# Kernel tuning notes

Hardware: AMD Instinct MI355X
Metric: run time of the kernel (lower is better)

Reference implementation:

```python
import jax, jax.numpy as jnp
import numpy as np

NEG_SLOPE = 0.2  # PyG GATConv default leaky_relu slope


def _gat_layer(x, W, att_src, att_dst, bias, src, dst, num_nodes, heads, out_c, concat):
    # x: [N, F_in] -> h: [N, H, C]
    h = (x @ W).reshape(num_nodes, heads, out_c)
    a_src = jnp.einsum('nhc,hc->nh', h, att_src)  # [N, H]
    a_dst = jnp.einsum('nhc,hc->nh', h, att_dst)  # [N, H]
    # edge (src -> dst): attention logit per edge/head
    e = jax.nn.leaky_relu(a_src[src] + a_dst[dst], NEG_SLOPE)  # [E, H]
    # softmax over edges sharing the same destination node
    m = jax.ops.segment_max(e, dst, num_segments=num_nodes)  # [N, H]
    m = jnp.where(jnp.isfinite(m), m, 0.0)
    ex = jnp.exp(e - m[dst])
    denom = jax.ops.segment_sum(ex, dst, num_segments=num_nodes)  # [N, H]
    alpha = ex / (denom[dst] + 1e-16)  # [E, H]
    # weighted scatter-add aggregation
    msg = h[src] * alpha[:, :, None]  # [E, H, C]
    out = jax.ops.segment_sum(msg, dst, num_segments=num_nodes)  # [N, H, C]
    if concat:
        out = out.reshape(num_nodes, heads * out_c)
    else:
        out = out.mean(axis=1)
    return out + bias


def _add_self_loops(edge_index, num_nodes):
    loop = jnp.arange(num_nodes, dtype=edge_index.dtype)
    src = jnp.concatenate([edge_index[0], loop])
    dst = jnp.concatenate([edge_index[1], loop])
    return src, dst


def setup_inputs() -> dict:
    key = jax.random.key(0)
    ks = jax.random.split(key, 9)
    N, F_in, E, H, C, OUT = 30000, 256, 300000, 8, 128, 64
    x = jax.random.normal(ks[0], (N, F_in), dtype=jnp.float32)
    edge_index = jax.random.randint(ks[1], (2, E), 0, N, dtype=jnp.int32)
    s1 = 1.0 / np.sqrt(F_in)
    s2 = 1.0 / np.sqrt(H * C)
    return {
        'x': x,
        'edge_index': edge_index,
        'W1': jax.random.normal(ks[2], (F_in, H * C), dtype=jnp.float32) * s1,
        'att_src1': jax.random.normal(ks[3], (H, C), dtype=jnp.float32) * s2,
        'att_dst1': jax.random.normal(ks[4], (H, C), dtype=jnp.float32) * s2,
        'b1': jnp.zeros((H * C,), dtype=jnp.float32),
        'W2': jax.random.normal(ks[5], (H * C, OUT), dtype=jnp.float32) * s2,
        'att_src2': jax.random.normal(ks[6], (1, OUT), dtype=jnp.float32) * 0.125,
        'att_dst2': jax.random.normal(ks[7], (1, OUT), dtype=jnp.float32) * 0.125,
        'b2': jnp.zeros((OUT,), dtype=jnp.float32),
    }


def reference(x, edge_index, W1, att_src1, att_dst1, b1, W2, att_src2, att_dst2, b2):
    N = x.shape[0]
    src, dst = _add_self_loops(edge_index, N)
    # dropout layers are identity in eval mode
    h = _gat_layer(x, W1, att_src1, att_dst1, b1, src, dst, N, 8, 128, True)
    h = jax.nn.elu(h)
    out = _gat_layer(h, W2, att_src2, att_dst2, b2, src, dst, N, 1, 64, False)
    return jax.nn.log_softmax(out, axis=-1)
```

## Files before the change

kernel.cpp:

```cpp
#include <hip/hip_runtime.h>
#include <math.h>

#define N_NODES 30000
#define F_IN 256
#define E_RAW 300000
#define E_TOT (E_RAW + N_NODES)
#define HEADS 8
#define CH 128
#define HC 1024
#define OUTC 64
#define NEG_SLOPE 0.2f
#define CAP 64

typedef __attribute__((ext_vector_type(8))) short bf16x8;
typedef __attribute__((ext_vector_type(4))) float f32x4;
typedef __attribute__((ext_vector_type(2))) float f32x2;

__device__ __forceinline__ float bf2f(unsigned short u) {
    return __uint_as_float(((unsigned)u) << 16);
}
__device__ __forceinline__ unsigned short f2bf(float f) {
    unsigned b = __float_as_uint(f);
    b += 0x7FFFu + ((b >> 16) & 1u);
    return (unsigned short)(b >> 16);
}
__device__ __forceinline__ void edge_sd(const int* __restrict__ ei, int e, int& s, int& d) {
    if (e < E_RAW) { s = ei[e]; d = ei[E_RAW + e]; }
    else           { s = e - E_RAW; d = s; }
}
__device__ __forceinline__ void async_cp16(const void* g, void* l) {
    __builtin_amdgcn_global_load_lds((const __attribute__((address_space(1))) void*)g,
                                     (__attribute__((address_space(3))) void*)l, 16, 0, 0);
}
__device__ __forceinline__ int slotP(int s) {
    return ((s >> 6) << 6) + ((s >> 2) & 15) + ((s & 3) << 4);
}
__device__ __forceinline__ void wave_sync() {
    __builtin_amdgcn_fence(__ATOMIC_ACQ_REL, "wavefront");
    __builtin_amdgcn_wave_barrier();
}

#define NB_CVTX (N_NODES * F_IN / 4 / 256)
#define NB_DEG  ((E_TOT + 255) / 256)
#define NB_W1T  ((F_IN * HC + 255) / 256)
#define NB_W2T  ((HC * OUTC + 255) / 256)
#define NB_PREP (NB_CVTX + NB_DEG + NB_W1T + NB_W2T)

__global__ __launch_bounds__(256)
void prep_kernel(const float* __restrict__ x, unsigned short* __restrict__ xb,
                 const float* __restrict__ W1, unsigned short* __restrict__ W1t,
                 const float* __restrict__ W2, unsigned short* __restrict__ W2t,
                 const int* __restrict__ ei, int* __restrict__ deg)
{
    const int b = blockIdx.x, t = threadIdx.x;
    if (b < NB_CVTX) {
        int i = b * 256 + t;
        const float4 v = reinterpret_cast<const float4*>(x)[i];
        ushort4 o;
        o.x = f2bf(v.x); o.y = f2bf(v.y); o.z = f2bf(v.z); o.w = f2bf(v.w);
        reinterpret_cast<ushort4*>(xb)[i] = o;
    } else if (b < NB_CVTX + NB_DEG) {
        int e = (b - NB_CVTX) * 256 + t;
        if (e < E_TOT) {
            int s, d; edge_sd(ei, e, s, d);
            atomicAdd(&deg[d], 1);
        }
    } else if (b < NB_CVTX + NB_DEG + NB_W1T) {
        int i = (b - NB_CVTX - NB_DEG) * 256 + t;
        if (i < F_IN * HC) {
            int k = i >> 10, n = i & (HC - 1);
            W1t[n * F_IN + k] = f2bf(W1[i]);
        }
    } else {
        int i = (b - NB_CVTX - NB_DEG - NB_W1T) * 256 + t;
        if (i < HC * OUTC) {
            int s = i >> 6, n = i & (OUTC - 1);
            W2t[n * HC + s] = f2bf(W2[slotP(s) * OUTC + n]);
        }
    }
}

__global__ __launch_bounds__(256)
void gemm1_mfma(const unsigned short* __restrict__ A,
                const unsigned short* __restrict__ Bt,
                unsigned* __restrict__ Cp,
                const float* __restrict__ att_src, const float* __restrict__ att_dst,
                float* __restrict__ a_src, float* __restrict__ a_dst, int M)
{
    __shared__ unsigned short Al[128 * 64];
    __shared__ unsigned short Bl[128 * 64];
    __shared__ float s_src[128][2];
    __shared__ float s_dst[128][2];
    const int tid  = threadIdx.x;
    const int wave = tid >> 6, lane = tid & 63;
    const int quad = lane >> 4, l16 = lane & 15;
    const int wr = (wave >> 1) * 64, wc = (wave & 1) * 64;
    const int row0 = blockIdx.y * 128;
    const int col0 = blockIdx.x * 128;

    f32x4 acc[4][4];
#pragma unroll
    for (int i = 0; i < 4; i++)
#pragma unroll
        for (int j = 0; j < 4; j++) acc[i][j] = (f32x4){0.f, 0.f, 0.f, 0.f};

    for (int k0 = 0; k0 < F_IN; k0 += 64) {
#pragma unroll
        for (int p = 0; p < 4; p++) {
            int idx = tid + 256 * p;
            int r = idx >> 3, q = idx & 7;
            async_cp16(A + (size_t)(row0 + r) * F_IN + k0 + ((q ^ (r & 7)) * 8),
                       Al + (size_t)(wave * 64 + 256 * p) * 8);
        }
#pragma unroll
        for (int p = 0; p < 4; p++) {
            int idx = tid + 256 * p;
            int r = idx >> 3, q = idx & 7;
            async_cp16(Bt + (size_t)(col0 + r) * F_IN + k0 + ((q ^ (r & 7)) * 8),
                       Bl + (size_t)(wave * 64 + 256 * p) * 8);
        }
        __syncthreads();
#pragma unroll
        for (int kh = 0; kh < 2; kh++) {
            const int cx = (kh * 4 + quad) ^ (l16 & 7);
            bf16x8 af[4], bg[4];
#pragma unroll
            for (int i = 0; i < 4; i++)
                af[i] = *reinterpret_cast<const bf16x8*>(Al + ((wr + i * 16 + l16) * 8 + cx) * 8);
#pragma unroll
            for (int j = 0; j < 4; j++)
                bg[j] = *reinterpret_cast<const bf16x8*>(Bl + ((wc + j * 16 + l16) * 8 + cx) * 8);
#pragma unroll
            for (int i = 0; i < 4; i++)
#pragma unroll
                for (int j = 0; j < 4; j++)
                    acc[i][j] = __builtin_amdgcn_mfma_f32_16x16x32_bf16(af[i], bg[j], acc[i][j], 0, 0, 0);
        }
        __syncthreads();
    }
    const int D = ((col0 + wc) >> 6) * 16 + l16;
#pragma unroll
    for (int i = 0; i < 4; i++) {
#pragma unroll
        for (int r = 0; r < 4; r++) {
            int row = row0 + wr + i * 16 + quad * 4 + r;
            if (row >= M) continue;
            int w8 = __builtin_amdgcn_cvt_pk_fp8_f32(acc[i][0][r], acc[i][1][r], 0, false);
            w8 = __builtin_amdgcn_cvt_pk_fp8_f32(acc[i][2][r], acc[i][3][r], w8, true);
            Cp[(size_t)row * 256 + D] = (unsigned)w8;
        }
    }
    const float* asv = att_src + blockIdx.x * CH;
    const float* adv = att_dst + blockIdx.x * CH;
    float av[4], dv[4];
#pragma unroll
    for (int j = 0; j < 4; j++) {
        av[j] = asv[wc + j * 16 + l16];
        dv[j] = adv[wc + j * 16 + l16];
    }
#pragma unroll
    for (int i = 0; i < 4; i++) {
#pragma unroll
        for (int r = 0; r < 4; r++) {
            float ps = 0.f, pd = 0.f;
#pragma unroll
            for (int j = 0; j < 4; j++) {
                float cc = acc[i][j][r];
                ps += cc * av[j];
                pd += cc * dv[j];
            }
#pragma unroll
            for (int o = 1; o < 16; o <<= 1) {
                ps += __shfl_xor(ps, o);
                pd += __shfl_xor(pd, o);
            }
            if (l16 == 0) {
                int lr = wr + i * 16 + quad * 4 + r;
                s_src[lr][wc >> 6] = ps;
                s_dst[lr][wc >> 6] = pd;
            }
        }
    }
    __syncthreads();
    if (tid < 128) {
        int row = row0 + tid;
        if (row < M) {
            a_src[row * 8 + blockIdx.x] = s_src[tid][0] + s_src[tid][1];
            a_dst[row * 8 + blockIdx.x] = s_dst[tid][0] + s_dst[tid][1];
        }
    }
}

__global__ __launch_bounds__(256)
void gemm2_mfma(const unsigned short* __restrict__ A,
                const unsigned short* __restrict__ Bt,
                unsigned short* __restrict__ C,
                const float* __restrict__ att_src2, const float* __restrict__ att_dst2,
                float* __restrict__ a_src2, float* __restrict__ a_dst2, int M)
{
    __shared__ unsigned short Al[64 * 64];
    __shared__ unsigned short Bl[64 * 64];
    const int tid  = threadIdx.x;
    const int wave = tid >> 6, lane = tid & 63;
    const int quad = lane >> 4, l16 = lane & 15;
    const int wr = wave * 16;
    const int row0 = blockIdx.x * 64;

    f32x4 acc[4];
#pragma unroll
    for (int j = 0; j < 4; j++) acc[j] = (f32x4){0.f, 0.f, 0.f, 0.f};

    for (int k0 = 0; k0 < HC; k0 += 64) {
#pragma unroll
        for (int p = 0; p < 2; p++) {
            int idx = tid + 256 * p;
            int r = idx >> 3, q = idx & 7;
            async_cp16(A + (size_t)(row0 + r) * HC + k0 + ((q ^ (r & 7)) * 8),
                       Al + (size_t)(wave * 64 + 256 * p) * 8);
        }
#pragma unroll
        for (int p = 0; p < 2; p++) {
            int idx = tid + 256 * p;
            int r = idx >> 3, q = idx & 7;
            async_cp16(Bt + (size_t)r * HC + k0 + ((q ^ (r & 7)) * 8),
                       Bl + (size_t)(wave * 64 + 256 * p) * 8);
        }
        __syncthreads();
#pragma unroll
        for (int kh = 0; kh < 2; kh++) {
            const int cx = (kh * 4 + quad) ^ (l16 & 7);
            bf16x8 af, bg[4];
            af = *reinterpret_cast<const bf16x8*>(Al + ((wr + l16) * 8 + cx) * 8);
#pragma unroll
            for (int j = 0; j < 4; j++)
                bg[j] = *reinterpret_cast<const bf16x8*>(Bl + ((j * 16 + l16) * 8 + cx) * 8);
#pragma unroll
            for (int j = 0; j < 4; j++)
                acc[j] = __builtin_amdgcn_mfma_f32_16x16x32_bf16(af, bg[j], acc[j], 0, 0, 0);
        }
        __syncthreads();
    }
    float av[4], dv[4];
#pragma unroll
    for (int j = 0; j < 4; j++) {
        av[j] = att_src2[j * 16 + l16];
        dv[j] = att_dst2[j * 16 + l16];
    }
#pragma unroll
    for (int r = 0; r < 4; r++) {
        int row = row0 + wr + quad * 4 + r;
        float ps = 0.f, pd = 0.f;
#pragma unroll
        for (int j = 0; j < 4; j++) {
            float cc = acc[j][r];
            int col = j * 16 + l16;
            if (row < M) C[(size_t)row * OUTC + col] = f2bf(cc);
            ps += cc * av[j];
            pd += cc * dv[j];
        }
#pragma unroll
        for (int o = 1; o < 16; o <<= 1) {
            ps += __shfl_xor(ps, o);
            pd += __shfl_xor(pd, o);
        }
        if (l16 == 0 && row < M) {
            a_src2[row] = ps;
            a_dst2[row] = pd;
        }
    }
}

__global__ __launch_bounds__(256)
void alloc_kernel(const int* __restrict__ deg, int* __restrict__ rowstart,
                  int* __restrict__ cursor, int* __restrict__ counter)
{
    int d = blockIdx.x * 256 + threadIdx.x;
    int lane = threadIdx.x & 63;
    int v = (d < N_NODES) ? deg[d] : 0;
    int x = v;
#pragma unroll
    for (int o = 1; o < 64; o <<= 1) {
        int y = __shfl_up(x, o);
        if (lane >= o) x += y;
    }
    int excl = x - v;
    int total = __shfl(x, 63);
    int base = 0;
    if (lane == 63) base = atomicAdd(counter, total);
    base = __shfl(base, 63);
    if (d < N_NODES) {
        rowstart[d] = base + excl;
        cursor[d]   = base + excl;
    }
}

__global__ void scatter_kernel(const int* __restrict__ ei, int* __restrict__ cursor,
                               int* __restrict__ csr_src)
{
    int e = blockIdx.x * 256 + threadIdx.x;
    if (e >= E_TOT) return;
    int s, d; edge_sd(ei, e, s, d);
    int pos = atomicAdd(&cursor[d], 1);
    csr_src[pos] = s;
}

__global__ __launch_bounds__(256)
void agg1_fused(const int* __restrict__ rowstart, const int* __restrict__ degv,
                const int* __restrict__ csr_src,
                const unsigned* __restrict__ h1p,
                const float* __restrict__ a_src1, const float* __restrict__ a_dst1,
                const float* __restrict__ b1, unsigned short* __restrict__ out1)
{
    const int t   = threadIdx.x;
    const int sub = t >> 6;
    const int tl  = t & 63;
    const int h   = tl >> 3;
    const int d   = blockIdx.x * 4 + sub;

    __shared__ float exps[4][CAP * 8];
    __shared__ int   srcs[4][CAP];

    const int start = rowstart[d];
    const int deg   = degv[d];

    const float adst = a_dst1[d * 8 + h];
    const uint4* __restrict__ h1v = reinterpret_cast<const uint4*>(h1p);

    float denom_part = 0.f;
    float acc[16];
#pragma unroll
    for (int k = 0; k < 16; k++) acc[k] = 0.f;

    for (int c0 = 0; c0 < deg; c0 += CAP) {
        const int cend = min(deg - c0, CAP);
        for (int c = (tl & 7); c < cend; c += 8) {
            int s = csr_src[start + c0 + c];
            if (h == 0) srcs[sub][c] = s;
            float a = a_src1[s * 8 + h] + adst;
            float v = a > 0.f ? a : NEG_SLOPE * a;
            float ex = __expf(v);
            exps[sub][c * 8 + h] = ex;
            denom_part += ex;
        }
        wave_sync();
        {
            int   s_cur = srcs[sub][0];
            float w_cur = exps[sub][h];
            uint4 u_cur = h1v[(size_t)s_cur * 64 + tl];
            for (int c = 0; c < cend; c++) {
                int   s_nxt = 0; float w_nxt = 0.f; uint4 u_nxt;
                if (c + 1 < cend) {
                    s_nxt = srcs[sub][c + 1];
                    w_nxt = exps[sub][(c + 1) * 8 + h];
                    u_nxt = h1v[(size_t)s_nxt * 64 + tl];
                }
#pragma unroll
                for (int dw = 0; dw < 4; dw++) {
                    unsigned wd = (&u_cur.x)[dw];
                    f32x2 lo = __builtin_amdgcn_cvt_pk_f32_fp8((int)wd, false);
                    f32x2 hi = __builtin_amdgcn_cvt_pk_f32_fp8((int)wd, true);
                    acc[dw * 4 + 0] += w_cur * lo.x;
                    acc[dw * 4 + 1] += w_cur * lo.y;
                    acc[dw * 4 + 2] += w_cur * hi.x;
                    acc[dw * 4 + 3] += w_cur * hi.y;
                }
                s_cur = s_nxt; w_cur = w_nxt; u_cur = u_nxt;
            }
        }
        wave_sync();
    }
#pragma unroll
    for (int o = 1; o < 8; o <<= 1) denom_part += __shfl_xor(denom_part, o);
    const float dinv = 1.f / (denom_part + 1e-16f);

    unsigned short ov[16];
#pragma unroll
    for (int e = 0; e < 16; e++) {
        float v = acc[e] * dinv + b1[slotP(16 * tl + e)];
        v = v > 0.f ? v : __expf(v) - 1.f;
        ov[e] = f2bf(v);
    }
    uint4* op = reinterpret_cast<uint4*>(out1 + (size_t)d * HC + 16 * tl);
    op[0] = *reinterpret_cast<uint4*>(&ov[0]);
    op[1] = *reinterpret_cast<uint4*>(&ov[8]);
}

__global__ __launch_bounds__(256)
void agg2_lsm(const int* __restrict__ rowstart, const int* __restrict__ degv,
              const int* __restrict__ csr_src,
              const unsigned short* __restrict__ h2,
              const float* __restrict__ a_src2, const float* __restrict__ a_dst2,
              const float* __restrict__ b2, float* __restrict__ out)
{
    const int t = threadIdx.x;
    const int sub  = t >> 6;
    const int lane = t & 63;
    const int eo   = lane >> 4;
    const int cq   = lane & 15;
    const int d = blockIdx.x * 4 + sub;

    __shared__ float exs[4][CAP];
    __shared__ int   ss[4][CAP];

    const int start = rowstart[d];
    const int deg   = degv[d];

    const float adst = a_dst2[d];
    const uint2* __restrict__ h2v = reinterpret_cast<const uint2*>(h2);
    float denom_part = 0.f;
    float ax = 0.f, ay = 0.f, az = 0.f, aw = 0.f;

    for (int c0 = 0; c0 < deg; c0 += CAP) {
        const int cend = min(deg - c0, CAP);
        for (int c = lane; c < cend; c += 64) {
            int s = csr_src[start + c0 + c];
            ss[sub][c] = s;
            float a = a_src2[s] + adst;
            float v = a > 0.f ? a : NEG_SLOPE * a;
            float ex = __expf(v);
            exs[sub][c] = ex;
            denom_part += ex;
        }
        wave_sync();
        {
            int   cc = eo;
            float w0 = (cc < cend) ? exs[sub][cc] : 0.f;
            int   s0 = (cc < cend) ? ss[sub][cc] : ss[sub][0];
            uint2 u0 = h2v[(size_t)s0 * 16 + cq];
            for (int c = 0; c + 4 < cend; c += 4) {
                int cc1 = c + 4 + eo;
                float w1 = (cc1 < cend) ? exs[sub][cc1] : 0.f;
                int   s1 = (cc1 < cend) ? ss[sub][cc1] : ss[sub][0];
                uint2 u1 = h2v[(size_t)s1 * 16 + cq];
                ax += w0 * __uint_as_float(u0.x << 16);
                ay += w0 * __uint_as_float(u0.x & 0xFFFF0000u);
                az += w0 * __uint_as_float(u0.y << 16);
                aw += w0 * __uint_as_float(u0.y & 0xFFFF0000u);
                w0 = w1; s0 = s1; u0 = u1;
            }
            ax += w0 * __uint_as_float(u0.x << 16);
            ay += w0 * __uint_as_float(u0.x & 0xFFFF0000u);
            az += w0 * __uint_as_float(u0.y << 16);
            aw += w0 * __uint_as_float(u0.y & 0xFFFF0000u);
        }
        wave_sync();
    }
    ax += __shfl_xor(ax, 16); ax += __shfl_xor(ax, 32);
    ay += __shfl_xor(ay, 16); ay += __shfl_xor(ay, 32);
    az += __shfl_xor(az, 16); az += __shfl_xor(az, 32);
    aw += __shfl_xor(aw, 16); aw += __shfl_xor(aw, 32);
#pragma unroll
    for (int o = 32; o > 0; o >>= 1) denom_part += __shfl_xor(denom_part, o);
    const float dinv = 1.f / (denom_part + 1e-16f);

    float4 bb = reinterpret_cast<const float4*>(b2)[cq];
    float v0 = ax * dinv + bb.x;
    float v1 = ay * dinv + bb.y;
    float v2 = az * dinv + bb.z;
    float v3 = aw * dinv + bb.w;
    float m = fmaxf(fmaxf(v0, v1), fmaxf(v2, v3));
#pragma unroll
    for (int o = 1; o < 16; o <<= 1) m = fmaxf(m, __shfl_xor(m, o));
    float ex = __expf(v0 - m) + __expf(v1 - m) + __expf(v2 - m) + __expf(v3 - m);
    float ssum = ex;
#pragma unroll
    for (int o = 1; o < 16; o <<= 1) ssum += __shfl_xor(ssum, o);
    if (eo == 0) {
        float lg = __logf(ssum);
        reinterpret_cast<float4*>(out + (size_t)d * OUTC)[cq] =
            make_float4(v0 - m - lg, v1 - m - lg, v2 - m - lg, v3 - m - lg);
    }
}

extern "C" void kernel_launch(void* const* d_in, const int* in_sizes, int n_in,
                              void* d_out, int out_size, void* d_ws, size_t ws_size,
                              hipStream_t stream)
{
    const float* x   = (const float*)d_in[0];
    const int*   ei  = (const int*)d_in[1];
    const float* W1  = (const float*)d_in[2];
    const float* as1 = (const float*)d_in[3];
    const float* ad1 = (const float*)d_in[4];
    const float* b1  = (const float*)d_in[5];
    const float* W2  = (const float*)d_in[6];
    const float* as2 = (const float*)d_in[7];
    const float* ad2 = (const float*)d_in[8];
    const float* b2  = (const float*)d_in[9];

    char* p = (char*)d_ws;
    auto alloc = [&](size_t bytes) { char* r = p; p += (bytes + 255) & ~(size_t)255; return r; };

    char* region0 = (char*)alloc((size_t)N_NODES * HC * 2);
    unsigned* h1p = (unsigned*)region0;

    char* region1 = (char*)alloc((size_t)N_NODES * HC * 2);
    unsigned short* out1 = (unsigned short*)region1;
    unsigned short* xb   = (unsigned short*)region1;
    unsigned short* W1t  = (unsigned short*)(region1 + (size_t)N_NODES * F_IN * 2 + 256);

    unsigned short* W2t = (unsigned short*)alloc((size_t)OUTC * HC * 2);

    float* a_src1   = (float*)alloc((size_t)N_NODES * HEADS * 4);
    float* a_dst1   = (float*)alloc((size_t)N_NODES * HEADS * 4);
    int*   deg      = (int*)alloc((size_t)(N_NODES + 1) * 4);
    int*   counter  = deg + N_NODES;
    int*   rowstart = (int*)alloc((size_t)N_NODES * 4);
    int*   cursor   = (int*)alloc((size_t)N_NODES * 4);
    int*   csr_src  = (int*)alloc((size_t)E_TOT * 4);

    char* q = region0;
    auto alias = [&](size_t bytes) { char* r = q; q += (bytes + 255) & ~(size_t)255; return r; };
    unsigned short* h2 = (unsigned short*)alias((size_t)N_NODES * OUTC * 2);
    float* a_src2  = (float*)alias((size_t)N_NODES * 4);
    float* a_dst2  = (float*)alias((size_t)N_NODES * 4);

    hipMemsetAsync(deg, 0, (size_t)(N_NODES + 1) * 4, stream);

    prep_kernel<<<NB_PREP, 256, 0, stream>>>(x, xb, W1, W1t, W2, W2t, ei, deg);

    alloc_kernel<<<(N_NODES + 255) / 256, 256, 0, stream>>>(deg, rowstart, cursor, counter);
    scatter_kernel<<<(E_TOT + 255) / 256, 256, 0, stream>>>(ei, cursor, csr_src);

    gemm1_mfma<<<dim3(HC / 128, (N_NODES + 127) / 128), 256, 0, stream>>>(
        xb, W1t, h1p, as1, ad1, a_src1, a_dst1, N_NODES);
    agg1_fused<<<N_NODES / 4, 256, 0, stream>>>(rowstart, deg, csr_src, h1p, a_src1, a_dst1, b1, out1);

    gemm2_mfma<<<(N_NODES + 63) / 64, 256, 0, stream>>>(
        out1, W2t, h2, as2, ad2, a_src2, a_dst2, N_NODES);
    agg2_lsm<<<N_NODES / 4, 256, 0, stream>>>(rowstart, deg, csr_src, h2, a_src2, a_dst2, b2, (float*)d_out);
}
```

Measured before the change: 259.0 us.

## Stream agg1 edges with 4-wide register prefetch, dropping shared-memory staging

The layer-1 aggregation no longer runs a two-phase scheme that first computes per-edge exp weights into shared memory and then replays them. Each wave now walks the CSR row in groups of four edges, software-pipelined one group ahead for the feature and logit loads and two groups ahead for the source indices. Each lane recomputes its head's exp weight inline, so the wave syncs, the LDS traffic and the shuffle reduction of the denominator go away. The row start and degree are made wave-uniform with readfirstlane. The cost is redundant exp and logit loads across the 8 lanes that share a head, plus higher register pressure from holding eight uint4 loads in flight.

```diff
diff --git a/kernel.cpp b/kernel.cpp
--- a/kernel.cpp
+++ b/kernel.cpp
@@ -304,6 +304,55 @@
     csr_src[pos] = s;
 }
 
+struct SG4 { int s0, s1, s2, s3; };
+struct AU4 { float a0, a1, a2, a3; uint4 u0, u1, u2, u3; };
+
+__device__ __forceinline__ SG4 ld_s4(const int* __restrict__ csr_src,
+                                     int start, int base, int deg)
+{
+    SG4 g;
+    g.s0 = (base + 0 < deg) ? csr_src[start + base + 0] : -1;
+    g.s1 = (base + 1 < deg) ? csr_src[start + base + 1] : -1;
+    g.s2 = (base + 2 < deg) ? csr_src[start + base + 2] : -1;
+    g.s3 = (base + 3 < deg) ? csr_src[start + base + 3] : -1;
+    return g;
+}
+
+__device__ __forceinline__ AU4 ld_au4(const float* __restrict__ a_src1,
+                                      const uint4* __restrict__ h1v,
+                                      SG4 g, int h, int tl)
+{
+    AU4 r;
+    const uint4 z = make_uint4(0u, 0u, 0u, 0u);
+    if (g.s0 >= 0) { r.a0 = a_src1[g.s0 * 8 + h]; r.u0 = h1v[(size_t)g.s0 * 64 + tl]; }
+    else           { r.a0 = -1e30f; r.u0 = z; }
+    if (g.s1 >= 0) { r.a1 = a_src1[g.s1 * 8 + h]; r.u1 = h1v[(size_t)g.s1 * 64 + tl]; }
+    else           { r.a1 = -1e30f; r.u1 = z; }
+    if (g.s2 >= 0) { r.a2 = a_src1[g.s2 * 8 + h]; r.u2 = h1v[(size_t)g.s2 * 64 + tl]; }
+    else           { r.a2 = -1e30f; r.u2 = z; }
+    if (g.s3 >= 0) { r.a3 = a_src1[g.s3 * 8 + h]; r.u3 = h1v[(size_t)g.s3 * 64 + tl]; }
+    else           { r.a3 = -1e30f; r.u3 = z; }
+    return r;
+}
+
+#define AGG1_DW(wd_, k_) do { \
+    f32x2 lo_ = __builtin_amdgcn_cvt_pk_f32_fp8((int)(wd_), false); \
+    f32x2 hi_ = __builtin_amdgcn_cvt_pk_f32_fp8((int)(wd_), true);  \
+    acc[(k_) + 0] += w_ * lo_.x; \
+    acc[(k_) + 1] += w_ * lo_.y; \
+    acc[(k_) + 2] += w_ * hi_.x; \
+    acc[(k_) + 3] += w_ * hi_.y; \
+} while (0)
+
+#define AGG1_EDGE(aa, uu) do { \
+    float al_ = (aa) + adst; \
+    float v_ = al_ > 0.f ? al_ : NEG_SLOPE * al_; \
+    float w_ = __expf(v_); \
+    denom += w_; \
+    AGG1_DW((uu).x, 0); AGG1_DW((uu).y, 4); \
+    AGG1_DW((uu).z, 8); AGG1_DW((uu).w, 12); \
+} while (0)
+
 __global__ __launch_bounds__(256)
 void agg1_fused(const int* __restrict__ rowstart, const int* __restrict__ degv,
                 const int* __restrict__ csr_src,
@@ -317,61 +366,32 @@
     const int h   = tl >> 3;
     const int d   = blockIdx.x * 4 + sub;
 
-    __shared__ float exps[4][CAP * 8];
-    __shared__ int   srcs[4][CAP];
-
-    const int start = rowstart[d];
-    const int deg   = degv[d];
-
+    const int start = __builtin_amdgcn_readfirstlane(rowstart[d]);
+    const int deg   = __builtin_amdgcn_readfirstlane(degv[d]);
     const float adst = a_dst1[d * 8 + h];
     const uint4* __restrict__ h1v = reinterpret_cast<const uint4*>(h1p);
 
-    float denom_part = 0.f;
+    float denom = 0.f;
     float acc[16];
 #pragma unroll
     for (int k = 0; k < 16; k++) acc[k] = 0.f;
 
-    for (int c0 = 0; c0 < deg; c0 += CAP) {
-        const int cend = min(deg - c0, CAP);
-        for (int c = (tl & 7); c < cend; c += 8) {
-            int s = csr_src[start + c0 + c];
-            if (h == 0) srcs[sub][c] = s;
-            float a = a_src1[s * 8 + h] + adst;
-            float v = a > 0.f ? a : NEG_SLOPE * a;
-            float ex = __expf(v);
-            exps[sub][c * 8 + h] = ex;
-            denom_part += ex;
-        }
-        wave_sync();
-        {
-            int   s_cur = srcs[sub][0];
-            float w_cur = exps[sub][h];
-            uint4 u_cur = h1v[(size_t)s_cur * 64 + tl];
-            for (int c = 0; c < cend; c++) {
-                int   s_nxt = 0; float w_nxt = 0.f; uint4 u_nxt;
-                if (c + 1 < cend) {
-                    s_nxt = srcs[sub][c + 1];
-                    w_nxt = exps[sub][(c + 1) * 8 + h];
-                    u_nxt = h1v[(size_t)s_nxt * 64 + tl];
-                }
-#pragma unroll
-                for (int dw = 0; dw < 4; dw++) {
-                    unsigned wd = (&u_cur.x)[dw];
-                    f32x2 lo = __builtin_amdgcn_cvt_pk_f32_fp8((int)wd, false);
-                    f32x2 hi = __builtin_amdgcn_cvt_pk_f32_fp8((int)wd, true);
-                    acc[dw * 4 + 0] += w_cur * lo.x;
-                    acc[dw * 4 + 1] += w_cur * lo.y;
-                    acc[dw * 4 + 2] += w_cur * hi.x;
-                    acc[dw * 4 + 3] += w_cur * hi.y;
-                }
-                s_cur = s_nxt; w_cur = w_nxt; u_cur = u_nxt;
-            }
-        }
-        wave_sync();
-    }
-#pragma unroll
-    for (int o = 1; o < 8; o <<= 1) denom_part += __shfl_xor(denom_part, o);
-    const float dinv = 1.f / (denom_part + 1e-16f);
+    SG4 sgN = ld_s4(csr_src, start, 0, deg);
+    AU4 auC = ld_au4(a_src1, h1v, sgN, h, tl);
+    sgN = ld_s4(csr_src, start, 4, deg);
+
+#pragma unroll 2
+    for (int c = 0; c < deg; c += 4) {
+        AU4 auN = ld_au4(a_src1, h1v, sgN, h, tl);
+        sgN = ld_s4(csr_src, start, c + 8, deg);
+        AGG1_EDGE(auC.a0, auC.u0);
+        AGG1_EDGE(auC.a1, auC.u1);
+        AGG1_EDGE(auC.a2, auC.u2);
+        AGG1_EDGE(auC.a3, auC.u3);
+        auC = auN;
+    }
+
+    const float dinv = 1.f / (denom + 1e-16f);
 
     unsigned short ov[16];
 #pragma unroll
```

Measured after the change: 256.2 us. Within noise of the previous version (-1.0%).

## Rewrite agg1 as two-node-per-wave register pipeline with packed FMA and exp2

Applied to the files above, without the earlier changes.

The layer-1 aggregation kernel now processes two destination nodes per wave and drops the shared-memory staging of source indices and exponentials. It computes the edge weights inline in batches of four, software-pipelining the index loads and gathers two stages deep. Accumulation uses v_pk_fma_f32 on fp8-unpacked pairs. The attention logits are prescaled by log2(e) in gemm1 so exp2 can replace exp. This is meant to raise memory-level parallelism and cut LDS and sync overhead in the gather, at the cost of more registers and lower occupancy. The inner edge loop also no longer subtracts the segment max, the same as the code before.

```diff
diff --git a/kernel.cpp b/kernel.cpp
--- a/kernel.cpp
+++ b/kernel.cpp
@@ -11,6 +11,7 @@
 #define OUTC 64
 #define NEG_SLOPE 0.2f
 #define CAP 64
+#define LOG2E 1.44269504f
 
 typedef __attribute__((ext_vector_type(8))) short bf16x8;
 typedef __attribute__((ext_vector_type(4))) float f32x4;
@@ -38,6 +39,11 @@
 __device__ __forceinline__ void wave_sync() {
     __builtin_amdgcn_fence(__ATOMIC_ACQ_REL, "wavefront");
     __builtin_amdgcn_wave_barrier();
+}
+__device__ __forceinline__ f32x2 pk_fma(f32x2 a, f32x2 b, f32x2 c) {
+    f32x2 d;
+    asm("v_pk_fma_f32 %0, %1, %2, %3" : "=v"(d) : "v"(a), "v"(b), "v"(c));
+    return d;
 }
 
 #define NB_CVTX (N_NODES * F_IN / 4 / 256)
@@ -185,8 +191,8 @@
     if (tid < 128) {
         int row = row0 + tid;
         if (row < M) {
-            a_src[row * 8 + blockIdx.x] = s_src[tid][0] + s_src[tid][1];
-            a_dst[row * 8 + blockIdx.x] = s_dst[tid][0] + s_dst[tid][1];
+            a_src[row * 8 + blockIdx.x] = (s_src[tid][0] + s_src[tid][1]) * LOG2E;
+            a_dst[row * 8 + blockIdx.x] = (s_dst[tid][0] + s_dst[tid][1]) * LOG2E;
         }
     }
 }
@@ -304,6 +310,73 @@
     csr_src[pos] = s;
 }
 
+struct G4 { int s[4]; };
+struct V4 { float a[4]; uint4 u[4]; };
+
+__device__ __forceinline__ G4 g4_load(const int* __restrict__ csr, int start, int c, int degm1) {
+    G4 g;
+#pragma unroll
+    for (int j = 0; j < 4; j++) g.s[j] = csr[start + min(c + j, degm1)];
+    return g;
+}
+__device__ __forceinline__ V4 v4_load(const float* __restrict__ a_src1,
+                                      const uint4* __restrict__ h1v,
+                                      G4 g, int h, int tl) {
+    V4 r;
+#pragma unroll
+    for (int j = 0; j < 4; j++) {
+        r.a[j] = a_src1[g.s[j] * 8 + h];
+        r.u[j] = h1v[(size_t)g.s[j] * 64 + tl];
+    }
+    return r;
+}
+
+#define EDGE_PK(al_, uu_, dn_, A_) do { \
+    float v_ = fmaxf((al_), NEG_SLOPE * (al_)); \
+    float w_ = __builtin_amdgcn_exp2f(v_); \
+    (dn_) += w_; \
+    f32x2 w2_; w2_.x = w_; w2_.y = w_; \
+    (A_)[0] = pk_fma(__builtin_amdgcn_cvt_pk_f32_fp8((int)(uu_).x, false), w2_, (A_)[0]); \
+    (A_)[1] = pk_fma(__builtin_amdgcn_cvt_pk_f32_fp8((int)(uu_).x, true ), w2_, (A_)[1]); \
+    (A_)[2] = pk_fma(__builtin_amdgcn_cvt_pk_f32_fp8((int)(uu_).y, false), w2_, (A_)[2]); \
+    (A_)[3] = pk_fma(__builtin_amdgcn_cvt_pk_f32_fp8((int)(uu_).y, true ), w2_, (A_)[3]); \
+    (A_)[4] = pk_fma(__builtin_amdgcn_cvt_pk_f32_fp8((int)(uu_).z, false), w2_, (A_)[4]); \
+    (A_)[5] = pk_fma(__builtin_amdgcn_cvt_pk_f32_fp8((int)(uu_).z, true ), w2_, (A_)[5]); \
+    (A_)[6] = pk_fma(__builtin_amdgcn_cvt_pk_f32_fp8((int)(uu_).w, false), w2_, (A_)[6]); \
+    (A_)[7] = pk_fma(__builtin_amdgcn_cvt_pk_f32_fp8((int)(uu_).w, true ), w2_, (A_)[7]); \
+} while (0)
+
+#define CONS4(V_, ad_, dn_, A_) do { \
+    EDGE_PK((V_).a[0] + (ad_), (V_).u[0], dn_, A_); \
+    EDGE_PK((V_).a[1] + (ad_), (V_).u[1], dn_, A_); \
+    EDGE_PK((V_).a[2] + (ad_), (V_).u[2], dn_, A_); \
+    EDGE_PK((V_).a[3] + (ad_), (V_).u[3], dn_, A_); \
+} while (0)
+
+#define CONS4C(V_, c_, deg_, ad_, dn_, A_) do { \
+    float a0_ = ((c_) + 0 < (deg_)) ? (V_).a[0] + (ad_) : -1e30f; EDGE_PK(a0_, (V_).u[0], dn_, A_); \
+    float a1_ = ((c_) + 1 < (deg_)) ? (V_).a[1] + (ad_) : -1e30f; EDGE_PK(a1_, (V_).u[1], dn_, A_); \
+    float a2_ = ((c_) + 2 < (deg_)) ? (V_).a[2] + (ad_) : -1e30f; EDGE_PK(a2_, (V_).u[2], dn_, A_); \
+    float a3_ = ((c_) + 3 < (deg_)) ? (V_).a[3] + (ad_) : -1e30f; EDGE_PK(a3_, (V_).u[3], dn_, A_); \
+} while (0)
+
+__device__ __forceinline__ void agg1_epi(int d, int tl, const f32x2* acc, float dn,
+                                         const float* __restrict__ b1,
+                                         unsigned short* __restrict__ out1)
+{
+    const float dinv = 1.f / (dn + 1e-16f);
+    unsigned short ov[16];
+#pragma unroll
+    for (int e = 0; e < 16; e++) {
+        float v = ((e & 1) ? acc[e >> 1].y : acc[e >> 1].x) * dinv + b1[slotP(16 * tl + e)];
+        v = v > 0.f ? v : __expf(v) - 1.f;
+        ov[e] = f2bf(v);
+    }
+    uint4* op = reinterpret_cast<uint4*>(out1 + (size_t)d * HC + 16 * tl);
+    op[0] = *reinterpret_cast<uint4*>(&ov[0]);
+    op[1] = *reinterpret_cast<uint4*>(&ov[8]);
+}
+
 __global__ __launch_bounds__(256)
 void agg1_fused(const int* __restrict__ rowstart, const int* __restrict__ degv,
                 const int* __restrict__ csr_src,
@@ -315,74 +388,56 @@
     const int sub = t >> 6;
     const int tl  = t & 63;
     const int h   = tl >> 3;
-    const int d   = blockIdx.x * 4 + sub;
-
-    __shared__ float exps[4][CAP * 8];
-    __shared__ int   srcs[4][CAP];
-
-    const int start = rowstart[d];
-    const int deg   = degv[d];
-
-    const float adst = a_dst1[d * 8 + h];
+    const int dA  = blockIdx.x * 8 + sub;
+    const int dB  = dA + 4;
+
+    const int startA = __builtin_amdgcn_readfirstlane(rowstart[dA]);
+    const int degA   = __builtin_amdgcn_readfirstlane(degv[dA]);
+    const int startB = __builtin_amdgcn_readfirstlane(rowstart[dB]);
+    const int degB   = __builtin_amdgcn_readfirstlane(degv[dB]);
+    const int dmA = degA - 1, dmB = degB - 1;
+    const float adA = a_dst1[dA * 8 + h];
+    const float adB = a_dst1[dB * 8 + h];
     const uint4* __restrict__ h1v = reinterpret_cast<const uint4*>(h1p);
 
-    float denom_part = 0.f;
-    float acc[16];
-#pragma unroll
-    for (int k = 0; k < 16; k++) acc[k] = 0.f;
-
-    for (int c0 = 0; c0 < deg; c0 += CAP) {
-        const int cend = min(deg - c0, CAP);
-        for (int c = (tl & 7); c < cend; c += 8) {
-            int s = csr_src[start + c0 + c];
-            if (h == 0) srcs[sub][c] = s;
-            float a = a_src1[s * 8 + h] + adst;
-            float v = a > 0.f ? a : NEG_SLOPE * a;
-            float ex = __expf(v);
-            exps[sub][c * 8 + h] = ex;
-            denom_part += ex;
-        }
-        wave_sync();
-        {
-            int   s_cur = srcs[sub][0];
-            float w_cur = exps[sub][h];
-            uint4 u_cur = h1v[(size_t)s_cur * 64 + tl];
-            for (int c = 0; c < cend; c++) {
-                int   s_nxt = 0; float w_nxt = 0.f; uint4 u_nxt;
-                if (c + 1 < cend) {
-                    s_nxt = srcs[sub][c + 1];
-                    w_nxt = exps[sub][(c + 1) * 8 + h];
-                    u_nxt = h1v[(size_t)s_nxt * 64 + tl];
-                }
-#pragma unroll
-                for (int dw = 0; dw < 4; dw++) {
-                    unsigned wd = (&u_cur.x)[dw];
-                    f32x2 lo = __builtin_amdgcn_cvt_pk_f32_fp8((int)wd, false);
-                    f32x2 hi = __builtin_amdgcn_cvt_pk_f32_fp8((int)wd, true);
-                    acc[dw * 4 + 0] += w_cur * lo.x;
-                    acc[dw * 4 + 1] += w_cur * lo.y;
-                    acc[dw * 4 + 2] += w_cur * hi.x;
-                    acc[dw * 4 + 3] += w_cur * hi.y;
-                }
-                s_cur = s_nxt; w_cur = w_nxt; u_cur = u_nxt;
-            }
-        }
-        wave_sync();
-    }
-#pragma unroll
-    for (int o = 1; o < 8; o <<= 1) denom_part += __shfl_xor(denom_part, o);
-    const float dinv = 1.f / (denom_part + 1e-16f);
-
-    unsigned short ov[16];
-#pragma unroll
-    for (int e = 0; e < 16; e++) {
-        float v = acc[e] * dinv + b1[slotP(16 * tl + e)];
-        v = v > 0.f ? v : __expf(v) - 1.f;
-        ov[e] = f2bf(v);
-    }
-    uint4* op = reinterpret_cast<uint4*>(out1 + (size_t)d * HC + 16 * tl);
-    op[0] = *reinterpret_cast<uint4*>(&ov[0]);
-    op[1] = *reinterpret_cast<uint4*>(&ov[8]);
+    float dnA = 0.f, dnB = 0.f;
+    f32x2 accA[8], accB[8];
+#pragma unroll
+    for (int k = 0; k < 8; k++) {
+        accA[k] = (f32x2){0.f, 0.f};
+        accB[k] = (f32x2){0.f, 0.f};
+    }
+
+    G4 sA = g4_load(csr_src, startA, 0, dmA);
+    G4 sB = g4_load(csr_src, startB, 0, dmB);
+    V4 Ac = v4_load(a_src1, h1v, sA, h, tl);
+    V4 Bc = v4_load(a_src1, h1v, sB, h, tl);
+    G4 sA1 = g4_load(csr_src, startA, 4, dmA);
+    G4 sB1 = g4_load(csr_src, startB, 4, dmB);
+
+#pragma unroll 1
+    for (int c = 0; ; c += 4) {
+        if (c < degA) {
+            const bool more = (c + 4 < degA);
+            V4 An;
+            if (more) { An = v4_load(a_src1, h1v, sA1, h, tl); sA1 = g4_load(csr_src, startA, c + 8, dmA); }
+            if (c + 4 <= degA) { CONS4(Ac, adA, dnA, accA); }
+            else               { CONS4C(Ac, c, degA, adA, dnA, accA); }
+            if (more) Ac = An;
+        }
+        if (c < degB) {
+            const bool more = (c + 4 < degB);
+            V4 Bn;
+            if (more) { Bn = v4_load(a_src1, h1v, sB1, h, tl); sB1 = g4_load(csr_src, startB, c + 8, dmB); }
+            if (c + 4 <= degB) { CONS4(Bc, adB, dnB, accB); }
+            else               { CONS4C(Bc, c, degB, adB, dnB, accB); }
+            if (more) Bc = Bn;
+        }
+        if (c + 4 >= degA && c + 4 >= degB) break;
+    }
+
+    agg1_epi(dA, tl, accA, dnA, b1, out1);
+    agg1_epi(dB, tl, accB, dnB, b1, out1);
 }
 
 __global__ __launch_bounds__(256)
@@ -523,7 +578,7 @@
 
     gemm1_mfma<<<dim3(HC / 128, (N_NODES + 127) / 128), 256, 0, stream>>>(
         xb, W1t, h1p, as1, ad1, a_src1, a_dst1, N_NODES);
-    agg1_fused<<<N_NODES / 4, 256, 0, stream>>>(rowstart, deg, csr_src, h1p, a_src1, a_dst1, b1, out1);
+    agg1_fused<<<N_NODES / 8, 256, 0, stream>>>(rowstart, deg, csr_src, h1p, a_src1, a_dst1, b1, out1);
 
     gemm2_mfma<<<(N_NODES + 63) / 64, 256, 0, stream>>>(
         out1, W2t, h2, as2, ad2, a_src2, a_dst2, N_NODES);
```

After: 266.0 us. 1.03x slower.
